# Kernel tuning notes

Hardware: AMD Instinct MI355X
Metric: run time of the kernel (lower is better)

## Reference

```python
import jax, jax.numpy as jnp
import numpy as np

EMBED = 1024
HEADS = 16
HDIM = 64
FF = 4 * EMBED
EPS = 1e-5


def layer_norm(x, g, b):
    mu = jnp.mean(x, axis=-1, keepdims=True)
    var = jnp.var(x, axis=-1, keepdims=True)
    return (x - mu) * jax.lax.rsqrt(var + EPS) * g + b


def setup_inputs() -> dict:
    key = jax.random.key(0)
    ks = jax.random.split(key, 12)
    s = lambda fan_in: 1.0 / np.sqrt(fan_in)
    return {
        "x": jax.random.normal(ks[0], (2, 2048, EMBED), jnp.float32),
        "w_qkv": jax.random.uniform(ks[1], (EMBED, 3 * HEADS * HDIM), jnp.float32, -s(EMBED), s(EMBED)),
        "w_proj": jax.random.uniform(ks[2], (HEADS * HDIM, EMBED), jnp.float32, -s(HEADS * HDIM), s(HEADS * HDIM)),
        "b_proj": jax.random.uniform(ks[3], (EMBED,), jnp.float32, -s(HEADS * HDIM), s(HEADS * HDIM)),
        "w1": jax.random.uniform(ks[4], (EMBED, FF), jnp.float32, -s(EMBED), s(EMBED)),
        "b1": jax.random.uniform(ks[5], (FF,), jnp.float32, -s(EMBED), s(EMBED)),
        "w2": jax.random.uniform(ks[6], (FF, EMBED), jnp.float32, -s(FF), s(FF)),
        "b2": jax.random.uniform(ks[7], (EMBED,), jnp.float32, -s(FF), s(FF)),
        "g1": jnp.ones((EMBED,), jnp.float32),
        "be1": jnp.zeros((EMBED,), jnp.float32),
        "g2": jnp.ones((EMBED,), jnp.float32),
        "be2": jnp.zeros((EMBED,), jnp.float32),
    }


def reference(x, w_qkv, w_proj, b_proj, w1, b1, w2, b2, g1, be1, g2, be2):
    bs, seq, _ = x.shape
    # --- MHA on pre-norm ---
    h = layer_norm(x, g1, be1)
    qkv = h @ w_qkv  # [b, s, 3*H*D]
    qkv = qkv.reshape(bs, seq, HEADS, 3, HDIM)
    q = qkv[:, :, :, 0, :]  # [b, s, h, d]
    k = qkv[:, :, :, 1, :]
    v = qkv[:, :, :, 2, :]
    attn = jnp.einsum("bqhd,bkhd->bhqk", q, k) / np.sqrt(HDIM)
    causal = jnp.tril(jnp.ones((seq, seq), bool))
    attn = jnp.where(causal, attn, -jnp.inf)
    attn = jax.nn.softmax(attn, axis=-1)
    out = jnp.einsum("bhqk,bkhd->bhqd", attn, v)
    # Faithful to original bug: .view without transposing heads back.
    out = out.reshape(bs, seq, HEADS * HDIM)
    out = out @ w_proj + b_proj
    x = x + out
    # --- FFN on pre-norm ---
    h2 = layer_norm(x, g2, be2)
    ff = jax.nn.relu(h2 @ w1 + b1) @ w2 + b2
    return x + ff
```

## Files before the change

kernel.cpp:

```cpp
#include <hip/hip_runtime.h>
#include <cstdint>

#define EMBED 1024
#define HEADS 16
#define HDIM  64
#define SEQ   2048
#define BATCH 2
#define ROWS  (BATCH*SEQ)

typedef __bf16 bf16x8 __attribute__((ext_vector_type(8)));
typedef float  f32x4  __attribute__((ext_vector_type(4)));
typedef float  f32x16 __attribute__((ext_vector_type(16)));
typedef unsigned int uint32x2 __attribute__((ext_vector_type(2)));

__device__ __forceinline__ unsigned short f2bf(float f) {
    union { float f; uint32_t u; } v; v.f = f;
    uint32_t r = v.u + 0x7fffu + ((v.u >> 16) & 1u);
    return (unsigned short)(r >> 16);
}

__device__ __forceinline__ uint32_t cvtpk_bf16(float lo, float hi) {
    uint32_t r;
    asm("v_cvt_pk_bf16_f32 %0, %1, %2" : "=v"(r) : "v"(lo), "v"(hi));
    return r;
}

__device__ __forceinline__ float fexp2(float x) {
    float r;
    asm("v_exp_f32 %0, %1" : "=v"(r) : "v"(x));
    return r;
}

#define GLDS(src, dst) __builtin_amdgcn_global_load_lds( \
    (const __attribute__((address_space(1))) uint32_t*)(src), \
    (__attribute__((address_space(3))) uint32_t*)(dst), 16, 0, 0)

__global__ __launch_bounds__(256) void k_transpose_bf16(
    const float* __restrict__ in, unsigned short* __restrict__ out, int K, int N)
{
    __shared__ float tile[32][33];
    const int tx = threadIdx.x & 31, ty = threadIdx.x >> 5;
    const int n0 = blockIdx.x * 32, k0 = blockIdx.y * 32;
#pragma unroll
    for (int r = 0; r < 4; ++r)
        tile[ty + 8*r][tx] = in[(size_t)(k0 + ty + 8*r) * N + n0 + tx];
    __syncthreads();
#pragma unroll
    for (int r = 0; r < 4; ++r)
        out[(size_t)(n0 + ty + 8*r) * K + k0 + tx] = f2bf(tile[tx][ty + 8*r]);
}

__global__ __launch_bounds__(256) void k_layernorm(
    const float* __restrict__ x, const float* __restrict__ g, const float* __restrict__ b,
    unsigned short* __restrict__ h)
{
    const int row = blockIdx.x, t = threadIdx.x;
    float4 v = ((const float4*)(x + (size_t)row * EMBED))[t];
    float s = v.x + v.y + v.z + v.w;
    float q = v.x*v.x + v.y*v.y + v.z*v.z + v.w*v.w;
#pragma unroll
    for (int off = 32; off >= 1; off >>= 1) {
        s += __shfl_xor(s, off, 64);
        q += __shfl_xor(q, off, 64);
    }
    __shared__ float ss[4], sq[4];
    if ((t & 63) == 0) { ss[t >> 6] = s; sq[t >> 6] = q; }
    __syncthreads();
    s = ss[0] + ss[1] + ss[2] + ss[3];
    q = sq[0] + sq[1] + sq[2] + sq[3];
    const float mu  = s * (1.0f / EMBED);
    const float var = q * (1.0f / EMBED) - mu * mu;
    const float rs  = rsqrtf(var + 1e-5f);
    float4 gv = ((const float4*)g)[t];
    float4 bv = ((const float4*)b)[t];
    ushort4 o;
    o.x = f2bf((v.x - mu) * rs * gv.x + bv.x);
    o.y = f2bf((v.y - mu) * rs * gv.y + bv.y);
    o.z = f2bf((v.z - mu) * rs * gv.z + bv.z);
    o.w = f2bf((v.w - mu) * rs * gv.w + bv.w);
    ((ushort4*)(h + (size_t)row * EMBED))[t] = o;
}

template<int FLAGS, typename OutT>
__global__ __launch_bounds__(512) void k_gemm_bt(
    const unsigned short* __restrict__ A,
    const unsigned short* __restrict__ BT,
    const float* __restrict__ bias,
    const float* __restrict__ resid,
    OutT* __restrict__ C,
    int M, int N, int K)
{
    __shared__ uint4 ldsv[4096];
    char* aL = (char*)ldsv;
    char* bL = aL + 16384;
    const int t = threadIdx.x, l = t & 63, w = t >> 6;
    const int wr = w >> 1, wc = w & 1;
    const int g = l >> 4, c = l & 15;

    const int gx = gridDim.x;
    const int lin = blockIdx.y * gx + blockIdx.x;
    const int cpx = (gx * gridDim.y) >> 3;
    const int swz = (lin & 7) * cpx + (lin >> 3);
    const int row0 = (swz / gx) * 128, col0 = (swz % gx) * 128;

    const int swc = (((l & 7) ^ (l >> 3)) * 8);
    const int rA0 = w*16 + (l >> 3), rA1 = rA0 + 8;
    const unsigned short* aS0 = A  + (size_t)(row0 + rA0) * K + swc;
    const unsigned short* aS1 = A  + (size_t)(row0 + rA1) * K + swc;
    const unsigned short* bS0 = BT + (size_t)(col0 + rA0) * K + swc;
    const unsigned short* bS1 = BT + (size_t)(col0 + rA1) * K + swc;
    const int dst0 = w * 2048, dst1 = w * 2048 + 1024;

    f32x4 acc[2][4];
#pragma unroll
    for (int m = 0; m < 2; ++m)
#pragma unroll
        for (int n = 0; n < 4; ++n) acc[m][n] = f32x4{0.f, 0.f, 0.f, 0.f};

    auto stage = [&](int kt, int bo) {
        const size_t ko = (size_t)kt * 64;
        GLDS(aS0 + ko, aL + bo + dst0);
        GLDS(aS1 + ko, aL + bo + dst1);
        GLDS(bS0 + ko, bL + bo + dst0);
        GLDS(bS1 + ko, bL + bo + dst1);
    };
    auto compute = [&](int bo) {
#pragma unroll
        for (int ks = 0; ks < 2; ++ks) {
            const int chb = ((ks*4 + g) ^ (c & 7)) * 16;
            bf16x8 af[2], bfr[4];
#pragma unroll
            for (int m = 0; m < 2; ++m)
                af[m] = *(const bf16x8*)(aL + bo + (wr*32 + m*16 + c) * 128 + chb);
#pragma unroll
            for (int n = 0; n < 4; ++n)
                bfr[n] = *(const bf16x8*)(bL + bo + (wc*64 + n*16 + c) * 128 + chb);
            __builtin_amdgcn_s_setprio(1);
#pragma unroll
            for (int m = 0; m < 2; ++m)
#pragma unroll
                for (int n = 0; n < 4; ++n)
                    acc[m][n] = __builtin_amdgcn_mfma_f32_16x16x32_bf16(af[m], bfr[n], acc[m][n], 0, 0, 0);
            __builtin_amdgcn_s_setprio(0);
        }
    };

    const int nkt = K >> 6;
    stage(0, 0);
    int bufo = 0;
    for (int kt = 0; kt < nkt - 1; ++kt) {
        stage(kt + 1, bufo ^ 32768);
        asm volatile("s_waitcnt vmcnt(4)" ::: "memory");
        __builtin_amdgcn_s_barrier();
        compute(bufo);
        asm volatile("s_waitcnt lgkmcnt(0)" ::: "memory");
        __builtin_amdgcn_s_barrier();
        bufo ^= 32768;
    }
    asm volatile("s_waitcnt vmcnt(0)" ::: "memory");
    __builtin_amdgcn_s_barrier();
    compute(bufo);

#pragma unroll
    for (int m = 0; m < 2; ++m) {
        const int rb = row0 + wr*32 + m*16 + g*4;
#pragma unroll
        for (int n = 0; n < 4; ++n) {
            const int col = col0 + wc*64 + n*16 + c;
            float bv = 0.f;
            if constexpr ((FLAGS & 1) != 0) bv = bias[col];
#pragma unroll
            for (int j = 0; j < 4; ++j) {
                float v = acc[m][n][j] + bv;
                if constexpr ((FLAGS & 2) != 0) v = fmaxf(v, 0.f);
                if constexpr ((FLAGS & 4) != 0) v += resid[(size_t)(rb + j) * N + col];
                if constexpr (sizeof(OutT) == 2) C[(size_t)(rb + j) * N + col] = (OutT)f2bf(v);
                else                             C[(size_t)(rb + j) * N + col] = v;
            }
        }
    }
}

template<int FLAGS, typename OutT>
__global__ __launch_bounds__(512) __attribute__((amdgpu_waves_per_eu(2, 2)))
void k_gemm256(
    const unsigned short* __restrict__ A,
    const unsigned short* __restrict__ BT,
    const float* __restrict__ bias,
    OutT* __restrict__ C,
    unsigned short* __restrict__ Qo,
    unsigned short* __restrict__ Ko,
    unsigned short* __restrict__ Vo,
    int M, int N, int K)
{
    __shared__ uint4 ldsv[8192];
    char* base = (char*)ldsv;
    const int t = threadIdx.x, l = t & 63, w = t >> 6;
    const int wr = w >> 2, wc = w & 3;
    const int g = l >> 4, c = l & 15;

    const int gx = gridDim.x;
    const int lin = blockIdx.y * gx + blockIdx.x;
    const int cpx = (gx * gridDim.y) >> 3;
    const int swz = (lin & 7) * cpx + (lin >> 3);
    const int row0 = (swz / gx) * 256, col0 = (swz % gx) * 256;

    const int sr = l >> 3, sc = l & 7;
    const int swk = (sc ^ sr) * 8;
    const unsigned short* aSr = A  + (size_t)(row0 + w*32 + sr) * K + swk;
    const unsigned short* bSr = BT + (size_t)(col0 + w*32 + sr) * K + swk;

    f32x4 acc[8][4];
#pragma unroll
    for (int m = 0; m < 8; ++m)
#pragma unroll
        for (int n = 0; n < 4; ++n) acc[m][n] = f32x4{0.f, 0.f, 0.f, 0.f};

    auto stage = [&](int kt, int bo) {
        const size_t ko = (size_t)kt * 64;
#pragma unroll
        for (int i = 0; i < 4; ++i) {
            GLDS(aSr + ko + (size_t)(i*8) * K, base + bo + (w*4 + i)*1024);
            GLDS(bSr + ko + (size_t)(i*8) * K, base + bo + 32768 + (w*4 + i)*1024);
        }
    };

    const int nkt = K >> 6;
    stage(0, 0);
    asm volatile("s_waitcnt vmcnt(0)" ::: "memory");
    __builtin_amdgcn_s_barrier();
    int bufo = 0;
    for (int kt = 0; kt < nkt; ++kt) {
        if (kt + 1 < nkt) stage(kt + 1, bufo ^ 65536);
        bf16x8 bfr[4][2];
#pragma unroll
        for (int n = 0; n < 4; ++n)
#pragma unroll
            for (int ks = 0; ks < 2; ++ks) {
                const int r = wc*64 + n*16 + c;
                bfr[n][ks] = *(const bf16x8*)(base + bufo + 32768 + r*128
                                              + (((ks*4 + g) ^ (c & 7)) * 16));
            }
#pragma unroll
        for (int p = 0; p < 4; ++p) {
            bf16x8 af[2][2];
#pragma unroll
            for (int mi = 0; mi < 2; ++mi)
#pragma unroll
                for (int ks = 0; ks < 2; ++ks) {
                    const int r = wr*128 + (p*2 + mi)*16 + c;
                    af[mi][ks] = *(const bf16x8*)(base + bufo + r*128
                                                  + (((ks*4 + g) ^ (c & 7)) * 16));
                }
            __builtin_amdgcn_s_setprio(1);
#pragma unroll
            for (int ks = 0; ks < 2; ++ks)
#pragma unroll
                for (int mi = 0; mi < 2; ++mi)
#pragma unroll
                    for (int n = 0; n < 4; ++n)
                        acc[p*2 + mi][n] = __builtin_amdgcn_mfma_f32_16x16x32_bf16(
                            af[mi][ks], bfr[n][ks], acc[p*2 + mi][n], 0, 0, 0);
            __builtin_amdgcn_s_setprio(0);
        }
        if (kt + 1 < nkt) {
            asm volatile("s_waitcnt vmcnt(0)" ::: "memory");
            __builtin_amdgcn_s_barrier();
            bufo ^= 65536;
        }
    }

    if constexpr ((FLAGS & 8) != 0) {
#pragma unroll
        for (int m = 0; m < 8; ++m) {
            const int rb = row0 + wr*128 + m*16 + g*4;
            const int b  = rb >> 11;
            const int q0 = rb & 2047;
#pragma unroll
            for (int n = 0; n < 4; ++n) {
                const int col = col0 + wc*64 + n*16 + c;
                const int hh  = col / 192;
                const int rem = col - hh * 192;
                const int tt  = rem >> 6;
                const int d   = rem & 63;
                const int bhh = b * HEADS + hh;
                if (tt == 2) {
                    const int st_e = q0 >> 6, kk = q0 & 63;
                    const int f_e  = (d >> 5) * 4 + (kk >> 4);
                    const int ln_e = ((kk >> 3) & 1) * 32 + (d & 31);
                    const int e0   = kk & 7;
                    ushort4 o;
                    o.x = f2bf(acc[m][n][0]); o.y = f2bf(acc[m][n][1]);
                    o.z = f2bf(acc[m][n][2]); o.w = f2bf(acc[m][n][3]);
                    *(ushort4*)(Vo + (size_t)bhh * (SEQ*HDIM) + st_e*4096 + f_e*512 + ln_e*8 + e0) = o;
                } else if (tt == 1) {
                    const int st_e = q0 >> 6;
                    const int f_e  = ((q0 >> 5) & 1) * 4 + (d >> 4);
                    const int lq_e = q0 & 31;
                    const int ln_b = ((d >> 3) & 1) * 32;
                    const int e_e  = d & 7;
                    unsigned short* dst = Ko + (size_t)bhh * (SEQ*HDIM) + st_e*4096 + f_e*512
                                             + (ln_b + lq_e)*8 + e_e;
#pragma unroll
                    for (int j = 0; j < 4; ++j)
                        dst[j*8] = f2bf(acc[m][n][j]);
                } else {
                    unsigned short* dst = Qo + ((size_t)bhh * SEQ + q0) * HDIM + d;
#pragma unroll
                    for (int j = 0; j < 4; ++j)
                        dst[(size_t)j * HDIM] = f2bf(acc[m][n][j]);
                }
            }
        }
    } else {
#pragma unroll
        for (int m = 0; m < 8; ++m) {
            const int rb = row0 + wr*128 + m*16 + g*4;
#pragma unroll
            for (int n = 0; n < 4; ++n) {
                const int col = col0 + wc*64 + n*16 + c;
                float bv = 0.f;
                if constexpr ((FLAGS & 1) != 0) bv = bias[col];
#pragma unroll
                for (int j = 0; j < 4; ++j) {
                    float v = acc[m][n][j] + bv;
                    if constexpr ((FLAGS & 2) != 0) v = fmaxf(v, 0.f);
                    if constexpr (sizeof(OutT) == 2) C[(size_t)(rb + j) * N + col] = (OutT)f2bf(v);
                    else                             C[(size_t)(rb + j) * N + col] = v;
                }
            }
        }
    }
}

__global__ __launch_bounds__(512) __attribute__((amdgpu_waves_per_eu(2, 2)))
void k_attention(
    const unsigned short* __restrict__ Qb,
    const unsigned short* __restrict__ Kf,
    const unsigned short* __restrict__ Vf,
    unsigned short* __restrict__ out)
{
    const int t = threadIdx.x, l = t & 63, w = t >> 6;
    const int lq = l & 31, hi = l >> 5;
    const int bid = blockIdx.x;
    const int sbid = (bid & 7) * 32 + (bid >> 3);
    const int bh = sbid >> 3, j = sbid & 7;
    const int qb = (w < 4) ? (4*j + w) : (63 - 4*j - (w - 4));
    const int q  = qb * 32 + lq;

    const unsigned short* Qh  = Qb + (size_t)bh * SEQ * HDIM;
    const unsigned short* Kfh = Kf + (size_t)bh * SEQ * HDIM + l*8;
    const unsigned short* Vfh = Vf + (size_t)bh * SEQ * HDIM + l*8;

    const bf16x8 qf0 = *(const bf16x8*)(Qh + (size_t)q * HDIM      + hi*8);
    const bf16x8 qf1 = *(const bf16x8*)(Qh + (size_t)q * HDIM + 16 + hi*8);
    const bf16x8 qf2 = *(const bf16x8*)(Qh + (size_t)q * HDIM + 32 + hi*8);
    const bf16x8 qf3 = *(const bf16x8*)(Qh + (size_t)q * HDIM + 48 + hi*8);

    f32x16 oT0, oT1;
#pragma unroll
    for (int i = 0; i < 16; ++i) { oT0[i] = 0.f; oT1[i] = 0.f; }
    float lacc0 = 0.f, lacc1 = 0.f, lacc2 = 0.f, lacc3 = 0.f;
    const float kSc = 0.18033688011112042f;
    const int nst = (qb >> 1) + 1;

    bf16x8 kA0, kA1, kA2, kA3, kA4, kA5, kA6, kA7;
    bf16x8 kB0, kB1, kB2, kB3, kB4, kB5, kB6, kB7;

#define LOADK(stv, KF) do {                                                     \
    const unsigned short* kp_ = Kfh + (size_t)(stv) * 4096;                     \
    KF##0 = *(const bf16x8*)(kp_ +    0); KF##1 = *(const bf16x8*)(kp_ +  512); \
    KF##2 = *(const bf16x8*)(kp_ + 1024); KF##3 = *(const bf16x8*)(kp_ + 1536); \
    KF##4 = *(const bf16x8*)(kp_ + 2048); KF##5 = *(const bf16x8*)(kp_ + 2560); \
    KF##6 = *(const bf16x8*)(kp_ + 3072); KF##7 = *(const bf16x8*)(kp_ + 3584); \
} while (0)

#define STEP(stv, KF) do {                                                      \
    const int kv0_ = (stv) * 64;                                                \
    const unsigned short* vp_ = Vfh + (size_t)(stv) * 4096;                     \
    bf16x8 vf0_ = *(const bf16x8*)(vp_ +    0), vf1_ = *(const bf16x8*)(vp_ +  512); \
    bf16x8 vf2_ = *(const bf16x8*)(vp_ + 1024), vf3_ = *(const bf16x8*)(vp_ + 1536); \
    bf16x8 vf4_ = *(const bf16x8*)(vp_ + 2048), vf5_ = *(const bf16x8*)(vp_ + 2560); \
    bf16x8 vf6_ = *(const bf16x8*)(vp_ + 3072), vf7_ = *(const bf16x8*)(vp_ + 3584); \
    f32x16 sA_, sB_;                                                            \
    _Pragma("unroll")                                                           \
    for (int i = 0; i < 16; ++i) { sA_[i] = 0.f; sB_[i] = 0.f; }               \
    __builtin_amdgcn_s_setprio(1);                                              \
    sA_ = __builtin_amdgcn_mfma_f32_32x32x16_bf16(KF##0, qf0, sA_, 0, 0, 0);    \
    sA_ = __builtin_amdgcn_mfma_f32_32x32x16_bf16(KF##1, qf1, sA_, 0, 0, 0);    \
    sA_ = __builtin_amdgcn_mfma_f32_32x32x16_bf16(KF##2, qf2, sA_, 0, 0, 0);    \
    sA_ = __builtin_amdgcn_mfma_f32_32x32x16_bf16(KF##3, qf3, sA_, 0, 0, 0);    \
    sB_ = __builtin_amdgcn_mfma_f32_32x32x16_bf16(KF##4, qf0, sB_, 0, 0, 0);    \
    sB_ = __builtin_amdgcn_mfma_f32_32x32x16_bf16(KF##5, qf1, sB_, 0, 0, 0);    \
    sB_ = __builtin_amdgcn_mfma_f32_32x32x16_bf16(KF##6, qf2, sB_, 0, 0, 0);    \
    sB_ = __builtin_amdgcn_mfma_f32_32x32x16_bf16(KF##7, qf3, sB_, 0, 0, 0);    \
    __builtin_amdgcn_s_setprio(0);                                              \
    float p_[32];                                                               \
    if ((stv) == nst - 1) {                                                     \
        _Pragma("unroll")                                                       \
        for (int r = 0; r < 16; ++r) {                                          \
            const int key_ = kv0_ + (r & 3) + 8*(r >> 2) + 4*hi;                \
            p_[r]      = (key_      <= q) ? fexp2(sA_[r] * kSc) : 0.f;          \
            p_[16 + r] = (key_ + 32 <= q) ? fexp2(sB_[r] * kSc) : 0.f;          \
        }                                                                       \
    } else {                                                                    \
        _Pragma("unroll")                                                       \
        for (int r = 0; r < 16; ++r) {                                          \
            p_[r]      = fexp2(sA_[r] * kSc);                                   \
            p_[16 + r] = fexp2(sB_[r] * kSc);                                   \
        }                                                                       \
    }                                                                           \
    _Pragma("unroll")                                                           \
    for (int i = 0; i < 32; i += 4) {                                           \
        lacc0 += p_[i]; lacc1 += p_[i+1]; lacc2 += p_[i+2]; lacc3 += p_[i+3];   \
    }                                                                           \
    bf16x8 pa_[4];                                                              \
    _Pragma("unroll")                                                           \
    for (int ks = 0; ks < 4; ++ks) {                                            \
        const int b8_ = ks * 8;                                                 \
        uint32x2 rA_ = __builtin_amdgcn_permlane32_swap(                        \
            cvtpk_bf16(p_[b8_+0], p_[b8_+1]), cvtpk_bf16(p_[b8_+4], p_[b8_+5]), false, false); \
        uint32x2 rB_ = __builtin_amdgcn_permlane32_swap(                        \
            cvtpk_bf16(p_[b8_+2], p_[b8_+3]), cvtpk_bf16(p_[b8_+6], p_[b8_+7]), false, false); \
        union { uint32_t u[4]; bf16x8 v; } pk_;                                 \
        pk_.u[0] = rA_[0]; pk_.u[1] = rB_[0]; pk_.u[2] = rA_[1]; pk_.u[3] = rB_[1]; \
        pa_[ks] = pk_.v;                                                        \
    }                                                                           \
    __builtin_amdgcn_s_setprio(1);                                              \
    oT0 = __builtin_amdgcn_mfma_f32_32x32x16_bf16(vf0_, pa_[0], oT0, 0, 0, 0);  \
    oT0 = __builtin_amdgcn_mfma_f32_32x32x16_bf16(vf1_, pa_[1], oT0, 0, 0, 0);  \
    oT0 = __builtin_amdgcn_mfma_f32_32x32x16_bf16(vf2_, pa_[2], oT0, 0, 0, 0);  \
    oT0 = __builtin_amdgcn_mfma_f32_32x32x16_bf16(vf3_, pa_[3], oT0, 0, 0, 0);  \
    oT1 = __builtin_amdgcn_mfma_f32_32x32x16_bf16(vf4_, pa_[0], oT1, 0, 0, 0);  \
    oT1 = __builtin_amdgcn_mfma_f32_32x32x16_bf16(vf5_, pa_[1], oT1, 0, 0, 0);  \
    oT1 = __builtin_amdgcn_mfma_f32_32x32x16_bf16(vf6_, pa_[2], oT1, 0, 0, 0);  \
    oT1 = __builtin_amdgcn_mfma_f32_32x32x16_bf16(vf7_, pa_[3], oT1, 0, 0, 0);  \
    __builtin_amdgcn_s_setprio(0);                                              \
} while (0)

    LOADK(0, kA);
    int st = 0;
    for (;;) {
        if (st + 1 < nst) LOADK(st + 1, kB);
        STEP(st, kA);
        if (++st >= nst) break;
        if (st + 1 < nst) LOADK(st + 1, kA);
        STEP(st, kB);
        if (++st >= nst) break;
    }
#undef LOADK
#undef STEP

    float lsum = (lacc0 + lacc1) + (lacc2 + lacc3);
    lsum += __shfl_xor(lsum, 32, 64);
    const float inv = 1.f / lsum;
    unsigned short* ob = out + ((size_t)bh * SEQ + q) * HDIM;
#pragma unroll
    for (int m2 = 0; m2 < 4; ++m2) {
        ushort4 o0, o1;
        o0.x = f2bf(oT0[m2*4+0] * inv); o0.y = f2bf(oT0[m2*4+1] * inv);
        o0.z = f2bf(oT0[m2*4+2] * inv); o0.w = f2bf(oT0[m2*4+3] * inv);
        o1.x = f2bf(oT1[m2*4+0] * inv); o1.y = f2bf(oT1[m2*4+1] * inv);
        o1.z = f2bf(oT1[m2*4+2] * inv); o1.w = f2bf(oT1[m2*4+3] * inv);
        *(ushort4*)(ob +      m2*8 + hi*4) = o0;
        *(ushort4*)(ob + 32 + m2*8 + hi*4) = o1;
    }
}

extern "C" void kernel_launch(void* const* d_in, const int* in_sizes, int n_in,
                              void* d_out, int out_size, void* d_ws, size_t ws_size,
                              hipStream_t stream)
{
    (void)in_sizes; (void)n_in; (void)out_size; (void)ws_size;
    const float* x      = (const float*)d_in[0];
    const float* w_qkv  = (const float*)d_in[1];
    const float* w_proj = (const float*)d_in[2];
    const float* b_proj = (const float*)d_in[3];
    const float* w1     = (const float*)d_in[4];
    const float* b1     = (const float*)d_in[5];
    const float* w2     = (const float*)d_in[6];
    const float* b2     = (const float*)d_in[7];
    const float* g1     = (const float*)d_in[8];
    const float* be1    = (const float*)d_in[9];
    const float* g2     = (const float*)d_in[10];
    const float* be2    = (const float*)d_in[11];

    char* ws = (char*)d_ws;
    size_t o = 0;
    auto take = [&](size_t bytes) -> char* {
        char* p = ws + o;
        o += (bytes + 255) & ~(size_t)255;
        return p;
    };
    unsigned short* wqkvT  = (unsigned short*)take(3072ull * 1024 * 2);
    unsigned short* wprojT = (unsigned short*)take(1024ull * 1024 * 2);
    unsigned short* w1T    = (unsigned short*)take(4096ull * 1024 * 2);
    unsigned short* w2T    = (unsigned short*)take(1024ull * 4096 * 2);
    unsigned short* h      = (unsigned short*)take(4096ull * 1024 * 2);
    unsigned short* Qb     = (unsigned short*)take(4096ull * 1024 * 2);
    unsigned short* Kfb    = (unsigned short*)take(4096ull * 1024 * 2);
    unsigned short* Vfb    = (unsigned short*)take(4096ull * 1024 * 2);
    unsigned short* attno  = (unsigned short*)take(4096ull * 1024 * 2);
    float*          x2     = (float*)take(4096ull * 1024 * 4);
    unsigned short* f1     = Qb;

    k_transpose_bf16<<<dim3(96, 32),  256, 0, stream>>>(w_qkv,  wqkvT,  1024, 3072);
    k_transpose_bf16<<<dim3(32, 32),  256, 0, stream>>>(w_proj, wprojT, 1024, 1024);
    k_transpose_bf16<<<dim3(128, 32), 256, 0, stream>>>(w1,     w1T,    1024, 4096);
    k_transpose_bf16<<<dim3(32, 128), 256, 0, stream>>>(w2,     w2T,    4096, 1024);

    k_layernorm<<<4096, 256, 0, stream>>>(x, g1, be1, h);
    k_gemm256<8, unsigned short><<<dim3(12, 16), 512, 0, stream>>>(
        h, wqkvT, nullptr, (unsigned short*)nullptr, Qb, Kfb, Vfb, ROWS, 3072, 1024);
    k_attention<<<256, 512, 0, stream>>>(Qb, Kfb, Vfb, attno);
    k_gemm_bt<5, float><<<dim3(8, 32), 512, 0, stream>>>(
        attno, wprojT, b_proj, x, x2, ROWS, 1024, 1024);
    k_layernorm<<<4096, 256, 0, stream>>>(x2, g2, be2, h);
    k_gemm256<3, unsigned short><<<dim3(16, 16), 512, 0, stream>>>(
        h, w1T, b1, f1, nullptr, nullptr, nullptr, ROWS, 4096, 1024);
    k_gemm_bt<5, float><<<dim3(8, 32), 512, 0, stream>>>(
        f1, w2T, b2, x2, (float*)d_out, ROWS, 1024, 4096);
}
```

Measured before the change: 188.5 us.

## Split K across wave halves in 128x128 GEMM with LDS reduction

Changes the 8-wave work split in k_gemm_bt. Previously each wave computed a 32x64 output tile over the full K slice of each 64-wide tile. Now four wave positions each own a 64x64 tile, and the two wave groups each handle one half of every K tile. The halves are reduced through LDS before the epilogue. Per-wave fragment reuse improves (4x4 MFMAs per loaded A/B set), at the cost of twice the accumulator registers, an extra LDS reduction pass, and only half the waves doing the epilogue.

```diff
diff --git a/kernel.cpp b/kernel.cpp
--- a/kernel.cpp
+++ b/kernel.cpp
@@ -91,10 +91,12 @@
     int M, int N, int K)
 {
     __shared__ uint4 ldsv[4096];
-    char* aL = (char*)ldsv;
-    char* bL = aL + 16384;
+    char* base = (char*)ldsv;
+    char* aL = base;
+    char* bL = base + 16384;
     const int t = threadIdx.x, l = t & 63, w = t >> 6;
-    const int wr = w >> 1, wc = w & 1;
+    const int pos = w & 3, kh = w >> 2;
+    const int qr = pos >> 1, qc = pos & 1;
     const int g = l >> 4, c = l & 15;
 
     const int gx = gridDim.x;
@@ -111,9 +113,9 @@
     const unsigned short* bS1 = BT + (size_t)(col0 + rA1) * K + swc;
     const int dst0 = w * 2048, dst1 = w * 2048 + 1024;
 
-    f32x4 acc[2][4];
-#pragma unroll
-    for (int m = 0; m < 2; ++m)
+    f32x4 acc[4][4];
+#pragma unroll
+    for (int m = 0; m < 4; ++m)
 #pragma unroll
         for (int n = 0; n < 4; ++n) acc[m][n] = f32x4{0.f, 0.f, 0.f, 0.f};
 
@@ -125,24 +127,21 @@
         GLDS(bS1 + ko, bL + bo + dst1);
     };
     auto compute = [&](int bo) {
-#pragma unroll
-        for (int ks = 0; ks < 2; ++ks) {
-            const int chb = ((ks*4 + g) ^ (c & 7)) * 16;
-            bf16x8 af[2], bfr[4];
-#pragma unroll
-            for (int m = 0; m < 2; ++m)
-                af[m] = *(const bf16x8*)(aL + bo + (wr*32 + m*16 + c) * 128 + chb);
+        const int chb = ((kh*4 + g) ^ (c & 7)) * 16;
+        bf16x8 af[4], bfr[4];
+#pragma unroll
+        for (int m = 0; m < 4; ++m)
+            af[m] = *(const bf16x8*)(aL + bo + (qr*64 + m*16 + c) * 128 + chb);
+#pragma unroll
+        for (int n = 0; n < 4; ++n)
+            bfr[n] = *(const bf16x8*)(bL + bo + (qc*64 + n*16 + c) * 128 + chb);
+        __builtin_amdgcn_s_setprio(1);
+#pragma unroll
+        for (int m = 0; m < 4; ++m)
 #pragma unroll
             for (int n = 0; n < 4; ++n)
-                bfr[n] = *(const bf16x8*)(bL + bo + (wc*64 + n*16 + c) * 128 + chb);
-            __builtin_amdgcn_s_setprio(1);
-#pragma unroll
-            for (int m = 0; m < 2; ++m)
-#pragma unroll
-                for (int n = 0; n < 4; ++n)
-                    acc[m][n] = __builtin_amdgcn_mfma_f32_16x16x32_bf16(af[m], bfr[n], acc[m][n], 0, 0, 0);
-            __builtin_amdgcn_s_setprio(0);
-        }
+                acc[m][n] = __builtin_amdgcn_mfma_f32_16x16x32_bf16(af[m], bfr[n], acc[m][n], 0, 0, 0);
+        __builtin_amdgcn_s_setprio(0);
     };
 
     const int nkt = K >> 6;
@@ -161,21 +160,36 @@
     __builtin_amdgcn_s_barrier();
     compute(bufo);
 
-#pragma unroll
-    for (int m = 0; m < 2; ++m) {
-        const int rb = row0 + wr*32 + m*16 + g*4;
-#pragma unroll
-        for (int n = 0; n < 4; ++n) {
-            const int col = col0 + wc*64 + n*16 + c;
-            float bv = 0.f;
-            if constexpr ((FLAGS & 1) != 0) bv = bias[col];
-#pragma unroll
-            for (int j = 0; j < 4; ++j) {
-                float v = acc[m][n][j] + bv;
-                if constexpr ((FLAGS & 2) != 0) v = fmaxf(v, 0.f);
-                if constexpr ((FLAGS & 4) != 0) v += resid[(size_t)(rb + j) * N + col];
-                if constexpr (sizeof(OutT) == 2) C[(size_t)(rb + j) * N + col] = (OutT)f2bf(v);
-                else                             C[(size_t)(rb + j) * N + col] = v;
+    asm volatile("s_waitcnt lgkmcnt(0)" ::: "memory");
+    __builtin_amdgcn_s_barrier();
+    if (kh) {
+#pragma unroll
+        for (int m = 0; m < 4; ++m)
+#pragma unroll
+            for (int n = 0; n < 4; ++n)
+                *(f32x4*)(base + (((pos*16 + m*4 + n) * 64) + l) * 16) = acc[m][n];
+    }
+    asm volatile("s_waitcnt lgkmcnt(0)" ::: "memory");
+    __builtin_amdgcn_s_barrier();
+
+    if (!kh) {
+#pragma unroll
+        for (int m = 0; m < 4; ++m) {
+            const int rb = row0 + qr*64 + m*16 + g*4;
+#pragma unroll
+            for (int n = 0; n < 4; ++n) {
+                const f32x4 part = *(const f32x4*)(base + (((pos*16 + m*4 + n) * 64) + l) * 16);
+                const int col = col0 + qc*64 + n*16 + c;
+                float bv = 0.f;
+                if constexpr ((FLAGS & 1) != 0) bv = bias[col];
+#pragma unroll
+                for (int j = 0; j < 4; ++j) {
+                    float v = acc[m][n][j] + part[j] + bv;
+                    if constexpr ((FLAGS & 2) != 0) v = fmaxf(v, 0.f);
+                    if constexpr ((FLAGS & 4) != 0) v += resid[(size_t)(rb + j) * N + col];
+                    if constexpr (sizeof(OutT) == 2) C[(size_t)(rb + j) * N + col] = (OutT)f2bf(v);
+                    else                             C[(size_t)(rb + j) * N + col] = v;
+                }
             }
         }
     }
```

Result: no change. 187.8 us (-0.4%).
